# Optimization experiments

Measured on AMD Instinct MI355X. Metric: run time of the kernel, lower is better.

## Reference

```python
import jax, jax.numpy as jnp
import numpy as np

E = 32      # particle_embed_dim = q/k/v head out dim
G = 2       # nof_net_types (conv groups)
NEG_SLOPE = 0.01


def _glin(x, w, b, groups):
    """Grouped 1x1 conv on (M, C, 1, 1) == grouped linear.
    x: (M, Cin), w: (Cout, Cin//groups), b: (Cout,)."""
    M = x.shape[0]
    Cout = w.shape[0]
    xg = x.reshape(M, groups, -1)                 # (M, G, Cin/G)
    wg = w.reshape(groups, Cout // groups, -1)    # (G, Cout/G, Cin/G)
    y = jnp.einsum('mgi,goi->mgo', xg, wg).reshape(M, Cout)
    return y + b


def setup_inputs() -> dict:
    key = jax.random.key(0)
    ks = jax.random.split(key, 9)
    B, N = 32, 1024
    s = 0.05
    return {
        'x_e':   jax.random.normal(ks[0], (B, N, G * E), dtype=jnp.float32),
        'w_qkv': jax.random.normal(ks[1], (3 * G * E, E), dtype=jnp.float32) * s,
        'b_qkv': jax.random.normal(ks[2], (3 * G * E,), dtype=jnp.float32) * s,
        'w_h1':  jax.random.normal(ks[3], (G * E, 2 * E), dtype=jnp.float32) * s,
        'b_h1':  jax.random.normal(ks[4], (G * E,), dtype=jnp.float32) * s,
        'w_h10': jax.random.normal(ks[5], (G * E, E), dtype=jnp.float32) * s,
        'b_h10': jax.random.normal(ks[6], (G * E,), dtype=jnp.float32) * s,
        'w_h11': jax.random.normal(ks[7], (G * E, E), dtype=jnp.float32) * s,
        'b_h11': jax.random.normal(ks[8], (G * E,), dtype=jnp.float32) * s,
    }


def reference(x_e, w_qkv, b_qkv, w_h1, b_h1, w_h10, b_h10, w_h11, b_h11):
    B, N, D = x_e.shape                      # D = G*E = 64
    act = lambda z: jnp.where(z >= 0, z, NEG_SLOPE * z)

    # grouped 1x1-conv QKV projection
    qkv = _glin(x_e.reshape(B * N, D), w_qkv, b_qkv, G)        # (B*N, 3*G*E)
    qkv = qkv.reshape(B, N, G, 3, E).transpose(0, 2, 3, 1, 4)  # (B, G, 3, N, E)
    q, k, v = qkv[:, :, 0], qkv[:, :, 1], qkv[:, :, 2]         # each (B, G, N, E)

    # NOTE: module divides k by sqrt(E) and logits by sqrt(E) again -> 1/E total
    scale = 1.0 / E
    ip = jnp.einsum('bgne,bgme->bgnm', q, k) * scale           # (B, G, N, N)
    sip = jax.nn.softmax(ip, axis=-1)
    attn = jnp.einsum('bgnm,bgme->bgne', sip, v)               # (B, G, N, E)

    # concat pre-attention v with attention output, regroup per-particle
    x_xe = jnp.concatenate([v, attn], axis=3)                  # (B, G, N, 2E)
    x_xe = x_xe.transpose(0, 2, 1, 3).reshape(B * N, G * 2 * E)  # (B*N, 128)

    h = act(_glin(x_xe, w_h1, b_h1, G))
    h = act(_glin(h, w_h10, b_h10, G))
    h = act(_glin(h, w_h11, b_h11, G))
    return h.reshape(B * N, G * E, 1, 1)
```

## Files before the change

kernel.cpp:

```cpp
#include <hip/hip_runtime.h>

#define B_ 32
#define N_ 1024
#define NEG 0.01f
#define QSC (1.4426950408889634f/32.0f)

using half8  = __attribute__((ext_vector_type(8))) _Float16;
using half4  = __attribute__((ext_vector_type(4))) _Float16;
using half2  = __attribute__((ext_vector_type(2))) _Float16;
using fp16x2 = __attribute__((ext_vector_type(2))) __fp16;
using floatx4 = __attribute__((ext_vector_type(4))) float;

#if defined(__has_builtin)
#if __has_builtin(__builtin_amdgcn_exp2f)
#define EXP2(x) __builtin_amdgcn_exp2f(x)
#endif
#endif
#ifndef EXP2
#define EXP2(x) exp2f(x)
#endif

#define MFMA32 __builtin_amdgcn_mfma_f32_16x16x32_f16
#define MFMA16 __builtin_amdgcn_mfma_f32_16x16x16f16

__device__ inline half2 pkcvt(float a, float b) {
    fp16x2 r = __builtin_amdgcn_cvt_pkrtz(a, b);
    return __builtin_bit_cast(half2, r);
}

__device__ inline half8 cvt8(float4 a, float4 b) {
    half2 p0 = pkcvt(a.x, a.y);
    half2 p1 = pkcvt(a.z, a.w);
    half2 p2 = pkcvt(b.x, b.y);
    half2 p3 = pkcvt(b.z, b.w);
    half8 h = { p0[0],p0[1], p1[0],p1[1], p2[0],p2[1], p3[0],p3[1] };
    return h;
}

struct __align__(16) Smem {
    _Float16 wsh[96*36];
    float    bsh[96];
    _Float16 Kst[2][128*40];
    _Float16 Vtst[2][32*136];
    _Float16 qs[128*40];
    _Float16 xs[128*72];
    float bl1[32], bl10[32], bl11[32];
};

__global__ __launch_bounds__(512, 2) void fused_kernel(
    const float* __restrict__ x, const float* __restrict__ w_qkv, const float* __restrict__ b_qkv,
    const float* __restrict__ w_h1,  const float* __restrict__ b_h1,
    const float* __restrict__ w_h10, const float* __restrict__ b_h10,
    const float* __restrict__ w_h11, const float* __restrict__ b_h11,
    float* __restrict__ out)
{
    __shared__ Smem sm;
    int t = threadIdx.x;
    int bid = blockIdx.x;
    int xcd = bid & 7, j = bid >> 3;
    int bg = xcd*8 + (j >> 3);
    int qtile = j & 7;
    int b = bg >> 1, g = bg & 1;
    int qbase = qtile * 128;
    int lane = t & 63, w = t >> 6;
    int L15 = lane & 15, quad = lane >> 4;

    for (int idx = t; idx < 96*32; idx += 512) {
        int r = idx >> 5, c = idx & 31;
        float wv = w_qkv[(g*96 + r)*32 + c];
        sm.wsh[r*36 + c] = (_Float16)(r < 32 ? wv*QSC : wv);
    }
    if (t < 96) sm.bsh[t] = b_qkv[g*96 + t];
    if (t < 32) {
        sm.bl1[t]  = b_h1[g*32+t];
        sm.bl10[t] = b_h10[g*32+t];
        sm.bl11[t] = b_h11[g*32+t];
    }
    __syncthreads();

    half8 bwk[2], bwv[2];
    float bkv[2], bvv[2];
    #pragma unroll
    for (int et = 0; et < 2; et++) {
        bwk[et] = *(const half8*)&sm.wsh[(32 + et*16 + L15)*36 + quad*8];
        bwv[et] = *(const half8*)&sm.wsh[(64 + et*16 + L15)*36 + quad*8];
        bkv[et] = sm.bsh[32 + et*16 + L15];
        bvv[et] = sm.bsh[64 + et*16 + L15];
    }

    {
        const float* p = x + ((size_t)b*N_ + qbase + w*16 + L15)*64 + g*32 + quad*8;
        half8 axq = cvt8(*(const float4*)p, *(const float4*)(p + 4));
        #pragma unroll
        for (int et = 0; et < 2; et++) {
            half8 bwq = *(const half8*)&sm.wsh[(et*16 + L15)*36 + quad*8];
            float bq = sm.bsh[et*16 + L15] * QSC;
            floatx4 cq = {bq,bq,bq,bq};
            floatx4 dq = MFMA32(axq, bwq, cq, 0,0,0);
            #pragma unroll
            for (int r = 0; r < 4; r++)
                sm.qs[(w*16 + quad*4 + r)*40 + et*16 + L15] = (_Float16)dq[r];
        }
    }
    __syncthreads();
    half8 bq0 = *(const half8*)&sm.qs[(w*16 + L15)*40 + quad*8];

    float4 xf0, xf1;
    auto prefetch = [&](int tile) {
        const float* p = x + ((size_t)b*N_ + tile*128 + w*16 + L15)*64 + g*32 + quad*8;
        xf0 = *(const float4*)p;
        xf1 = *(const float4*)(p + 4);
    };
    auto proj_tile = [&](int tile, int buf) {
        half8 ax = cvt8(xf0, xf1);
        floatx4 dK[2], dV[2];
        #pragma unroll
        for (int et = 0; et < 2; et++) {
            floatx4 ck = {bkv[et],bkv[et],bkv[et],bkv[et]};
            floatx4 cv = {bvv[et],bvv[et],bvv[et],bvv[et]};
            dK[et] = MFMA32(ax, bwk[et], ck, 0,0,0);
            dV[et] = MFMA32(ax, bwv[et], cv, 0,0,0);
        }
        int rb = w*16 + quad*4;
        #pragma unroll
        for (int et = 0; et < 2; et++) {
            half2 k01 = pkcvt(dK[et][0], dK[et][1]);
            half2 k23 = pkcvt(dK[et][2], dK[et][3]);
            sm.Kst[buf][(rb+0)*40 + et*16 + L15] = k01[0];
            sm.Kst[buf][(rb+1)*40 + et*16 + L15] = k01[1];
            sm.Kst[buf][(rb+2)*40 + et*16 + L15] = k23[0];
            sm.Kst[buf][(rb+3)*40 + et*16 + L15] = k23[1];
            half2 v01 = pkcvt(dV[et][0], dV[et][1]);
            half2 v23 = pkcvt(dV[et][2], dV[et][3]);
            half4 vh = { v01[0], v01[1], v23[0], v23[1] };
            *(half4*)&sm.Vtst[buf][(et*16 + L15)*136 + rb] = vh;
            if (tile == qtile) {
                #pragma unroll
                for (int r = 0; r < 4; r++)
                    sm.xs[(rb + r)*72 + et*16 + L15] = vh[r];
            }
        }
    };

    prefetch(0);
    proj_tile(0, 0);
    __syncthreads();

    const floatx4 zz = {0.f,0.f,0.f,0.f};
    floatx4 o00 = zz, o01 = zz;
    float lsum0 = 0.f;

    for (int kt = 0; kt < 8; kt++) {
        int cur = kt & 1;
        if (kt < 7) prefetch(kt + 1);
        __builtin_amdgcn_s_setprio(1);
        #pragma unroll
        for (int m8 = 0; m8 < 8; m8++) {
            half8 ak = *(const half8*)&sm.Kst[cur][(m8*16 + L15)*40 + quad*8];
            floatx4 s0 = MFMA32(ak, bq0, zz, 0,0,0);
            float p00 = EXP2(s0.x), p01 = EXP2(s0.y), p02 = EXP2(s0.z), p03 = EXP2(s0.w);
            lsum0 += (p00+p01)+(p02+p03);
            half2 pa = pkcvt(p00, p01);
            half2 pb = pkcvt(p02, p03);
            half4 a0 = { pa[0], pa[1], pb[0], pb[1] };
            half4 bv0 = *(const half4*)&sm.Vtst[cur][      L15*136 + m8*16 + quad*4];
            half4 bv1 = *(const half4*)&sm.Vtst[cur][(16 + L15)*136 + m8*16 + quad*4];
            o00 = MFMA16(a0, bv0, o00, 0,0,0);
            o01 = MFMA16(a0, bv1, o01, 0,0,0);
        }
        __builtin_amdgcn_s_setprio(0);
        if (kt < 7) {
            proj_tile(kt + 1, 1 - cur);
            __syncthreads();
        }
    }

    lsum0 += __shfl_xor(lsum0, 16, 64);
    lsum0 += __shfl_xor(lsum0, 32, 64);
    float linv_own = 1.0f / lsum0;
    float li0 = __shfl(linv_own, quad*4 + 0, 64);
    float li1 = __shfl(linv_own, quad*4 + 1, 64);
    float li2 = __shfl(linv_own, quad*4 + 2, 64);
    float li3 = __shfl(linv_own, quad*4 + 3, 64);

    #pragma unroll
    for (int et = 0; et < 2; et++) {
        floatx4 ov = et ? o01 : o00;
        sm.xs[(w*16+quad*4+0)*72 + 32 + et*16 + L15] = (_Float16)(ov[0]*li0);
        sm.xs[(w*16+quad*4+1)*72 + 32 + et*16 + L15] = (_Float16)(ov[1]*li1);
        sm.xs[(w*16+quad*4+2)*72 + 32 + et*16 + L15] = (_Float16)(ov[2]*li2);
        sm.xs[(w*16+quad*4+3)*72 + 32 + et*16 + L15] = (_Float16)(ov[3]*li3);
    }

    half4 a1f[2][4], a2f[2][2], a3f[2][2];
    #pragma unroll
    for (int mt = 0; mt < 2; mt++) {
        #pragma unroll
        for (int kt = 0; kt < 4; kt++) {
            float4 f = *(const float4*)(w_h1 + (size_t)(g*32+mt*16+L15)*64 + kt*16 + quad*4);
            half2 ha = pkcvt(f.x, f.y);
            half2 hb = pkcvt(f.z, f.w);
            half4 hh = { ha[0], ha[1], hb[0], hb[1] };
            a1f[mt][kt] = hh;
        }
        #pragma unroll
        for (int kt = 0; kt < 2; kt++) {
            float4 f = *(const float4*)(w_h10 + (size_t)(g*32+mt*16+L15)*32 + kt*16 + quad*4);
            half2 ha = pkcvt(f.x, f.y);
            half2 hb = pkcvt(f.z, f.w);
            half4 hh = { ha[0], ha[1], hb[0], hb[1] };
            a2f[mt][kt] = hh;
            float4 f2 = *(const float4*)(w_h11 + (size_t)(g*32+mt*16+L15)*32 + kt*16 + quad*4);
            half2 hc = pkcvt(f2.x, f2.y);
            half2 hd = pkcvt(f2.z, f2.w);
            half4 h2 = { hc[0], hc[1], hd[0], hd[1] };
            a3f[mt][kt] = h2;
        }
    }

    floatx4 d1[2];
    #pragma unroll
    for (int mt = 0; mt < 2; mt++) {
        float4 bb = *(const float4*)&sm.bl1[mt*16 + quad*4];
        d1[mt] = (floatx4){bb.x, bb.y, bb.z, bb.w};
    }
    #pragma unroll
    for (int kt = 0; kt < 4; kt++) {
        half4 b1 = *(const half4*)&sm.xs[(w*16 + L15)*72 + kt*16 + quad*4];
        d1[0] = MFMA16(a1f[0][kt], b1, d1[0], 0,0,0);
        d1[1] = MFMA16(a1f[1][kt], b1, d1[1], 0,0,0);
    }
    half4 h1b[2];
    #pragma unroll
    for (int mt = 0; mt < 2; mt++) {
        float v0 = d1[mt][0]; v0 = (v0>=0.f)?v0:NEG*v0;
        float v1 = d1[mt][1]; v1 = (v1>=0.f)?v1:NEG*v1;
        float v2 = d1[mt][2]; v2 = (v2>=0.f)?v2:NEG*v2;
        float v3 = d1[mt][3]; v3 = (v3>=0.f)?v3:NEG*v3;
        half2 ha = pkcvt(v0, v1);
        half2 hb = pkcvt(v2, v3);
        half4 hh = { ha[0], ha[1], hb[0], hb[1] };
        h1b[mt] = hh;
    }
    floatx4 d2[2];
    #pragma unroll
    for (int mt = 0; mt < 2; mt++) {
        float4 bb = *(const float4*)&sm.bl10[mt*16 + quad*4];
        d2[mt] = (floatx4){bb.x, bb.y, bb.z, bb.w};
        #pragma unroll
        for (int kt = 0; kt < 2; kt++)
            d2[mt] = MFMA16(a2f[mt][kt], h1b[kt], d2[mt], 0,0,0);
    }
    half4 h2b[2];
    #pragma unroll
    for (int mt = 0; mt < 2; mt++) {
        float v0 = d2[mt][0]; v0 = (v0>=0.f)?v0:NEG*v0;
        float v1 = d2[mt][1]; v1 = (v1>=0.f)?v1:NEG*v1;
        float v2 = d2[mt][2]; v2 = (v2>=0.f)?v2:NEG*v2;
        float v3 = d2[mt][3]; v3 = (v3>=0.f)?v3:NEG*v3;
        half2 ha = pkcvt(v0, v1);
        half2 hb = pkcvt(v2, v3);
        half4 hh = { ha[0], ha[1], hb[0], hb[1] };
        h2b[mt] = hh;
    }
    floatx4 d3[2];
    #pragma unroll
    for (int mt = 0; mt < 2; mt++) {
        float4 bb = *(const float4*)&sm.bl11[mt*16 + quad*4];
        d3[mt] = (floatx4){bb.x, bb.y, bb.z, bb.w};
        #pragma unroll
        for (int kt = 0; kt < 2; kt++)
            d3[mt] = MFMA16(a3f[mt][kt], h2b[kt], d3[mt], 0,0,0);
    }
    #pragma unroll
    for (int mt = 0; mt < 2; mt++) {
        float4 ov;
        ov.x = d3[mt][0]; ov.x = (ov.x>=0.f)?ov.x:NEG*ov.x;
        ov.y = d3[mt][1]; ov.y = (ov.y>=0.f)?ov.y:NEG*ov.y;
        ov.z = d3[mt][2]; ov.z = (ov.z>=0.f)?ov.z:NEG*ov.z;
        ov.w = d3[mt][3]; ov.w = (ov.w>=0.f)?ov.w:NEG*ov.w;
        *(float4*)(out + ((size_t)b*N_ + qbase + w*16 + L15)*64 + g*32 + mt*16 + quad*4) = ov;
    }
}

extern "C" void kernel_launch(void* const* d_in, const int* in_sizes, int n_in,
                              void* d_out, int out_size, void* d_ws, size_t ws_size,
                              hipStream_t stream) {
    const float* x_e   = (const float*)d_in[0];
    const float* w_qkv = (const float*)d_in[1];
    const float* b_qkv = (const float*)d_in[2];
    const float* w_h1  = (const float*)d_in[3];
    const float* b_h1  = (const float*)d_in[4];
    const float* w_h10 = (const float*)d_in[5];
    const float* b_h10 = (const float*)d_in[6];
    const float* w_h11 = (const float*)d_in[7];
    const float* b_h11 = (const float*)d_in[8];
    float* out = (float*)d_out;

    hipLaunchKernelGGL(fused_kernel, dim3(B_*2*8), dim3(512), 0, stream,
                       x_e, w_qkv, b_qkv, w_h1, b_h1, w_h10, b_h10, w_h11, b_h11, out);
}
```

Before: 119.2 us.

## Start key loop at own query tile, fuse Q projection, alias smem buffers

The key/value loop now starts at the block's own query tile and wraps around. This lets Q, K and V come from a single x load and a single pass of MFMAs, which removes the separate Q projection, its extra global read and one barrier. The K bias is dropped because it is constant along the softmax axis, the K stride shrinks from 40 to 36, and the K/V staging buffers now share memory with the xs buffer through a union. Less LDS per block could raise occupancy, at the cost of an extra barrier before xs is reused and a possible change in LDS bank-conflict behaviour from the new stride.

```diff
diff --git a/kernel.cpp b/kernel.cpp
--- a/kernel.cpp
+++ b/kernel.cpp
@@ -40,10 +40,13 @@
 struct __align__(16) Smem {
     _Float16 wsh[96*36];
     float    bsh[96];
-    _Float16 Kst[2][128*40];
-    _Float16 Vtst[2][32*136];
-    _Float16 qs[128*40];
-    _Float16 xs[128*72];
+    union {
+        struct {
+            _Float16 Kst[2][128*36];
+            _Float16 Vtst[2][32*136];
+        } a;
+        _Float16 xs[128*72];
+    } u;
     float bl1[32], bl10[32], bl11[32];
 };
 
@@ -64,6 +67,7 @@
     int qbase = qtile * 128;
     int lane = t & 63, w = t >> 6;
     int L15 = lane & 15, quad = lane >> 4;
+    const floatx4 zz = {0.f,0.f,0.f,0.f};
 
     for (int idx = t; idx < 96*32; idx += 512) {
         int r = idx >> 5, c = idx & 31;
@@ -78,118 +82,126 @@
     }
     __syncthreads();
 
-    half8 bwk[2], bwv[2];
-    float bkv[2], bvv[2];
+    half8 bwq[2], bwk[2], bwv[2];
+    floatx4 cv[2];
     #pragma unroll
     for (int et = 0; et < 2; et++) {
+        bwq[et] = *(const half8*)&sm.wsh[(     et*16 + L15)*36 + quad*8];
         bwk[et] = *(const half8*)&sm.wsh[(32 + et*16 + L15)*36 + quad*8];
         bwv[et] = *(const half8*)&sm.wsh[(64 + et*16 + L15)*36 + quad*8];
-        bkv[et] = sm.bsh[32 + et*16 + L15];
-        bvv[et] = sm.bsh[64 + et*16 + L15];
-    }
-
-    {
-        const float* p = x + ((size_t)b*N_ + qbase + w*16 + L15)*64 + g*32 + quad*8;
-        half8 axq = cvt8(*(const float4*)p, *(const float4*)(p + 4));
-        #pragma unroll
-        for (int et = 0; et < 2; et++) {
-            half8 bwq = *(const half8*)&sm.wsh[(et*16 + L15)*36 + quad*8];
-            float bq = sm.bsh[et*16 + L15] * QSC;
-            floatx4 cq = {bq,bq,bq,bq};
-            floatx4 dq = MFMA32(axq, bwq, cq, 0,0,0);
-            #pragma unroll
-            for (int r = 0; r < 4; r++)
-                sm.qs[(w*16 + quad*4 + r)*40 + et*16 + L15] = (_Float16)dq[r];
-        }
-    }
-    __syncthreads();
-    half8 bq0 = *(const half8*)&sm.qs[(w*16 + L15)*40 + quad*8];
-
+        float bv = sm.bsh[64 + et*16 + L15];
+        cv[et] = (floatx4){bv,bv,bv,bv};
+    }
+
+    _Float16* qs = sm.u.a.Kst[1];
+
+    half4 vown[2];
     float4 xf0, xf1;
     auto prefetch = [&](int tile) {
         const float* p = x + ((size_t)b*N_ + tile*128 + w*16 + L15)*64 + g*32 + quad*8;
         xf0 = *(const float4*)p;
         xf1 = *(const float4*)(p + 4);
     };
-    auto proj_tile = [&](int tile, int buf) {
+    auto proj_tile = [&](int buf) {
         half8 ax = cvt8(xf0, xf1);
-        floatx4 dK[2], dV[2];
+        int rb = w*16 + quad*4;
         #pragma unroll
         for (int et = 0; et < 2; et++) {
-            floatx4 ck = {bkv[et],bkv[et],bkv[et],bkv[et]};
-            floatx4 cv = {bvv[et],bvv[et],bvv[et],bvv[et]};
-            dK[et] = MFMA32(ax, bwk[et], ck, 0,0,0);
-            dV[et] = MFMA32(ax, bwv[et], cv, 0,0,0);
-        }
+            floatx4 dk = MFMA32(ax, bwk[et], zz, 0,0,0);
+            floatx4 dv = MFMA32(ax, bwv[et], cv[et], 0,0,0);
+            half2 k01 = pkcvt(dk[0], dk[1]);
+            half2 k23 = pkcvt(dk[2], dk[3]);
+            sm.u.a.Kst[buf][(rb+0)*36 + et*16 + L15] = k01[0];
+            sm.u.a.Kst[buf][(rb+1)*36 + et*16 + L15] = k01[1];
+            sm.u.a.Kst[buf][(rb+2)*36 + et*16 + L15] = k23[0];
+            sm.u.a.Kst[buf][(rb+3)*36 + et*16 + L15] = k23[1];
+            half2 v01 = pkcvt(dv[0], dv[1]);
+            half2 v23 = pkcvt(dv[2], dv[3]);
+            half4 vh = { v01[0], v01[1], v23[0], v23[1] };
+            *(half4*)&sm.u.a.Vtst[buf][(et*16 + L15)*136 + rb] = vh;
+        }
+    };
+
+    prefetch(qtile);
+    {
+        half8 ax = cvt8(xf0, xf1);
         int rb = w*16 + quad*4;
         #pragma unroll
         for (int et = 0; et < 2; et++) {
-            half2 k01 = pkcvt(dK[et][0], dK[et][1]);
-            half2 k23 = pkcvt(dK[et][2], dK[et][3]);
-            sm.Kst[buf][(rb+0)*40 + et*16 + L15] = k01[0];
-            sm.Kst[buf][(rb+1)*40 + et*16 + L15] = k01[1];
-            sm.Kst[buf][(rb+2)*40 + et*16 + L15] = k23[0];
-            sm.Kst[buf][(rb+3)*40 + et*16 + L15] = k23[1];
-            half2 v01 = pkcvt(dV[et][0], dV[et][1]);
-            half2 v23 = pkcvt(dV[et][2], dV[et][3]);
+            float bq = sm.bsh[et*16 + L15] * QSC;
+            floatx4 cq = {bq,bq,bq,bq};
+            floatx4 dq = MFMA32(ax, bwq[et], cq, 0,0,0);
+            floatx4 dk = MFMA32(ax, bwk[et], zz, 0,0,0);
+            floatx4 dv = MFMA32(ax, bwv[et], cv[et], 0,0,0);
+            #pragma unroll
+            for (int r = 0; r < 4; r++)
+                qs[(rb+r)*36 + et*16 + L15] = (_Float16)dq[r];
+            half2 k01 = pkcvt(dk[0], dk[1]);
+            half2 k23 = pkcvt(dk[2], dk[3]);
+            sm.u.a.Kst[0][(rb+0)*36 + et*16 + L15] = k01[0];
+            sm.u.a.Kst[0][(rb+1)*36 + et*16 + L15] = k01[1];
+            sm.u.a.Kst[0][(rb+2)*36 + et*16 + L15] = k23[0];
+            sm.u.a.Kst[0][(rb+3)*36 + et*16 + L15] = k23[1];
+            half2 v01 = pkcvt(dv[0], dv[1]);
+            half2 v23 = pkcvt(dv[2], dv[3]);
             half4 vh = { v01[0], v01[1], v23[0], v23[1] };
-            *(half4*)&sm.Vtst[buf][(et*16 + L15)*136 + rb] = vh;
-            if (tile == qtile) {
-                #pragma unroll
-                for (int r = 0; r < 4; r++)
-                    sm.xs[(rb + r)*72 + et*16 + L15] = vh[r];
-            }
-        }
-    };
-
-    prefetch(0);
-    proj_tile(0, 0);
+            *(half4*)&sm.u.a.Vtst[0][(et*16 + L15)*136 + rb] = vh;
+            vown[et] = vh;
+        }
+    }
+    half8 bq0 = *(const half8*)&qs[(w*16 + L15)*36 + quad*8];
     __syncthreads();
 
-    const floatx4 zz = {0.f,0.f,0.f,0.f};
     floatx4 o00 = zz, o01 = zz;
     float lsum0 = 0.f;
 
     for (int kt = 0; kt < 8; kt++) {
         int cur = kt & 1;
-        if (kt < 7) prefetch(kt + 1);
+        if (kt < 7) prefetch((qtile + kt + 1) & 7);
         __builtin_amdgcn_s_setprio(1);
         #pragma unroll
         for (int m8 = 0; m8 < 8; m8++) {
-            half8 ak = *(const half8*)&sm.Kst[cur][(m8*16 + L15)*40 + quad*8];
+            half8 ak = *(const half8*)&sm.u.a.Kst[cur][(m8*16 + L15)*36 + quad*8];
             floatx4 s0 = MFMA32(ak, bq0, zz, 0,0,0);
             float p00 = EXP2(s0.x), p01 = EXP2(s0.y), p02 = EXP2(s0.z), p03 = EXP2(s0.w);
             lsum0 += (p00+p01)+(p02+p03);
             half2 pa = pkcvt(p00, p01);
             half2 pb = pkcvt(p02, p03);
             half4 a0 = { pa[0], pa[1], pb[0], pb[1] };
-            half4 bv0 = *(const half4*)&sm.Vtst[cur][      L15*136 + m8*16 + quad*4];
-            half4 bv1 = *(const half4*)&sm.Vtst[cur][(16 + L15)*136 + m8*16 + quad*4];
+            half4 bv0 = *(const half4*)&sm.u.a.Vtst[cur][      L15*136 + m8*16 + quad*4];
+            half4 bv1 = *(const half4*)&sm.u.a.Vtst[cur][(16 + L15)*136 + m8*16 + quad*4];
             o00 = MFMA16(a0, bv0, o00, 0,0,0);
             o01 = MFMA16(a0, bv1, o01, 0,0,0);
         }
         __builtin_amdgcn_s_setprio(0);
         if (kt < 7) {
-            proj_tile(kt + 1, 1 - cur);
+            proj_tile(1 - cur);
             __syncthreads();
         }
     }
+    __syncthreads();
 
     lsum0 += __shfl_xor(lsum0, 16, 64);
     lsum0 += __shfl_xor(lsum0, 32, 64);
-    float linv_own = 1.0f / lsum0;
-    float li0 = __shfl(linv_own, quad*4 + 0, 64);
-    float li1 = __shfl(linv_own, quad*4 + 1, 64);
-    float li2 = __shfl(linv_own, quad*4 + 2, 64);
-    float li3 = __shfl(linv_own, quad*4 + 3, 64);
-
-    #pragma unroll
-    for (int et = 0; et < 2; et++) {
-        floatx4 ov = et ? o01 : o00;
-        sm.xs[(w*16+quad*4+0)*72 + 32 + et*16 + L15] = (_Float16)(ov[0]*li0);
-        sm.xs[(w*16+quad*4+1)*72 + 32 + et*16 + L15] = (_Float16)(ov[1]*li1);
-        sm.xs[(w*16+quad*4+2)*72 + 32 + et*16 + L15] = (_Float16)(ov[2]*li2);
-        sm.xs[(w*16+quad*4+3)*72 + 32 + et*16 + L15] = (_Float16)(ov[3]*li3);
+    float inv0 = 1.0f / lsum0;
+    float li[4];
+    #pragma unroll
+    for (int r = 0; r < 4; r++)
+        li[r] = __shfl(inv0, quad*4 + r, 64);
+
+    {
+        int rb = w*16 + quad*4;
+        #pragma unroll
+        for (int et = 0; et < 2; et++) {
+            #pragma unroll
+            for (int r = 0; r < 4; r++)
+                sm.u.xs[(rb+r)*72 + et*16 + L15] = vown[et][r];
+            floatx4 ov = et ? o01 : o00;
+            sm.u.xs[(rb+0)*72 + 32 + et*16 + L15] = (_Float16)(ov[0]*li[0]);
+            sm.u.xs[(rb+1)*72 + 32 + et*16 + L15] = (_Float16)(ov[1]*li[1]);
+            sm.u.xs[(rb+2)*72 + 32 + et*16 + L15] = (_Float16)(ov[2]*li[2]);
+            sm.u.xs[(rb+3)*72 + 32 + et*16 + L15] = (_Float16)(ov[3]*li[3]);
+        }
     }
 
     half4 a1f[2][4], a2f[2][2], a3f[2][2];
@@ -200,16 +212,16 @@
             float4 f = *(const float4*)(w_h1 + (size_t)(g*32+mt*16+L15)*64 + kt*16 + quad*4);
             half2 ha = pkcvt(f.x, f.y);
             half2 hb = pkcvt(f.z, f.w);
-            half4 hh = { ha[0], ha[1], hb[0], hb[1] };
-            a1f[mt][kt] = hh;
+            half4 h = { ha[0], ha[1], hb[0], hb[1] };
+            a1f[mt][kt] = h;
         }
         #pragma unroll
         for (int kt = 0; kt < 2; kt++) {
             float4 f = *(const float4*)(w_h10 + (size_t)(g*32+mt*16+L15)*32 + kt*16 + quad*4);
             half2 ha = pkcvt(f.x, f.y);
             half2 hb = pkcvt(f.z, f.w);
-            half4 hh = { ha[0], ha[1], hb[0], hb[1] };
-            a2f[mt][kt] = hh;
+            half4 h = { ha[0], ha[1], hb[0], hb[1] };
+            a2f[mt][kt] = h;
             float4 f2 = *(const float4*)(w_h11 + (size_t)(g*32+mt*16+L15)*32 + kt*16 + quad*4);
             half2 hc = pkcvt(f2.x, f2.y);
             half2 hd = pkcvt(f2.z, f2.w);
@@ -226,7 +238,7 @@
     }
     #pragma unroll
     for (int kt = 0; kt < 4; kt++) {
-        half4 b1 = *(const half4*)&sm.xs[(w*16 + L15)*72 + kt*16 + quad*4];
+        half4 b1 = *(const half4*)&sm.u.xs[(w*16 + L15)*72 + kt*16 + quad*4];
         d1[0] = MFMA16(a1f[0][kt], b1, d1[0], 0,0,0);
         d1[1] = MFMA16(a1f[1][kt], b1, d1[1], 0,0,0);
     }
@@ -239,8 +251,8 @@
         float v3 = d1[mt][3]; v3 = (v3>=0.f)?v3:NEG*v3;
         half2 ha = pkcvt(v0, v1);
         half2 hb = pkcvt(v2, v3);
-        half4 hh = { ha[0], ha[1], hb[0], hb[1] };
-        h1b[mt] = hh;
+        half4 h = { ha[0], ha[1], hb[0], hb[1] };
+        h1b[mt] = h;
     }
     floatx4 d2[2];
     #pragma unroll
@@ -260,8 +272,8 @@
         float v3 = d2[mt][3]; v3 = (v3>=0.f)?v3:NEG*v3;
         half2 ha = pkcvt(v0, v1);
         half2 hb = pkcvt(v2, v3);
-        half4 hh = { ha[0], ha[1], hb[0], hb[1] };
-        h2b[mt] = hh;
+        half4 h = { ha[0], ha[1], hb[0], hb[1] };
+        h2b[mt] = h;
     }
     floatx4 d3[2];
     #pragma unroll
```

Result: faster. 101.0 us (-15.3%).
